# Kernel optimization log

Hardware: AMD Instinct MI355X
Metric: run time of the kernel (lower is better)

Reference implementation:

```python
import jax, jax.numpy as jnp
import numpy as np

NUM_HEAD = 8
D_MODEL = 512
HEAD_DIM = D_MODEL // NUM_HEAD
SCALING = HEAD_DIM ** (-0.5)
B, NQ, NK = 2, 2048, 2048


def setup_inputs() -> dict:
    key = jax.random.key(0)
    ks = jax.random.split(key, 12)
    s = 1.0 / np.sqrt(D_MODEL)
    return {
        "q": jax.random.normal(ks[0], (B, NQ, D_MODEL), jnp.float32),
        "k": jax.random.normal(ks[1], (B, NK, D_MODEL), jnp.float32),
        "v": jax.random.normal(ks[2], (B, NK, D_MODEL), jnp.float32),
        "mask_head": jax.random.uniform(ks[3], (B, NUM_HEAD, NQ, NK), jnp.float32),
        "pearson_matrix": jax.random.normal(ks[4], (B, NUM_HEAD, NK, NK), jnp.float32),
        "Wq": jax.random.uniform(ks[5], (D_MODEL, D_MODEL), jnp.float32, -s, s),
        "bq": jax.random.uniform(ks[6], (D_MODEL,), jnp.float32, -s, s),
        "Wk": jax.random.uniform(ks[7], (D_MODEL, D_MODEL), jnp.float32, -s, s),
        "bk": jax.random.uniform(ks[8], (D_MODEL,), jnp.float32, -s, s),
        "Wv": jax.random.uniform(ks[9], (D_MODEL, D_MODEL), jnp.float32, -s, s),
        "bv": jax.random.uniform(ks[10], (D_MODEL,), jnp.float32, -s, s),
    }


def _split_heads(x):
    b, n, _ = x.shape
    return x.reshape(b, n, NUM_HEAD, HEAD_DIM).transpose(0, 2, 1, 3)  # b h n d


def reference(q, k, v, mask_head, pearson_matrix, Wq, bq, Wk, bk, Wv, bv):
    queries = _split_heads(q @ Wq.T + bq)
    keys = _split_heads(k @ Wk.T + bk)
    values = _split_heads(v @ Wv.T + bv)
    energy = jnp.einsum('bhqd,bhkd->bhqk', queries, keys) * SCALING
    att = jax.nn.softmax(energy, axis=-1)
    att = att * mask_head
    # einsum 'bhqk,bhkk->bhqk' = multiply by diagonal of pearson over last two axes
    diag = jnp.diagonal(pearson_matrix, axis1=-2, axis2=-1)  # b h k
    att = att * diag[:, :, None, :]
    agg = jnp.einsum('bhqk,bhkd->bhqd', att, values)
    b, h, n, d = agg.shape
    return agg.transpose(0, 2, 1, 3).reshape(b, n, h * d)
```

## Files before the change

### kernel.cpp

```cpp
#include <hip/hip_runtime.h>

#define NUM_HEAD 8
#define D_MODEL  512
#define HEAD_DIM 64
#define NSEQ     2048
#define SCALE_LOG2E 0.18033688011112042f

typedef __attribute__((ext_vector_type(8))) short bf16x8;
typedef __attribute__((ext_vector_type(4))) float f32x4;

static __device__ __forceinline__ unsigned short f2bf(float f) {
    unsigned u = __builtin_bit_cast(unsigned, f);
    u += 0x7fffu + ((u >> 16) & 1u);
    return (unsigned short)(u >> 16);
}
static __device__ __forceinline__ float bf2f(unsigned short h) {
    unsigned u = ((unsigned)h) << 16;
    return __builtin_bit_cast(float, u);
}
static __device__ __forceinline__ unsigned pk2(float a, float b) {
    return (unsigned)f2bf(a) | ((unsigned)f2bf(b) << 16);
}

#define PSTR 40

__global__ __launch_bounds__(256) void proj_kernel(
    const float* __restrict__ X, const float* __restrict__ W,
    const float* __restrict__ bias, unsigned short* __restrict__ outp)
{
    __shared__ unsigned short lA[128 * PSTR];
    __shared__ unsigned short lB[64 * PSTR];

    const int tid  = threadIdx.x;
    const int lane = tid & 63, wid = tid >> 6;
    const int quad = lane >> 4, l15 = lane & 15;
    const int wm = (wid >> 1) * 64;
    const int wn = (wid & 1) * 32;
    const int m0 = blockIdx.x * 128, n0 = blockIdx.y * 64;

    f32x4 acc[4][2];
    const f32x4 zf = {0.f, 0.f, 0.f, 0.f};
#pragma unroll
    for (int mi = 0; mi < 4; mi++)
#pragma unroll
        for (int ni = 0; ni < 2; ni++) acc[mi][ni] = zf;

    const int arow = tid >> 1, akc = (tid & 1) * 16;
    const int brow = tid >> 2, bkc = (tid & 3) * 8;

    for (int k0 = 0; k0 < D_MODEL; k0 += 32) {
        const float* ap = X + (m0 + arow) * D_MODEL + k0 + akc;
        float4 a0 = *(const float4*)(ap);
        float4 a1 = *(const float4*)(ap + 4);
        float4 a2 = *(const float4*)(ap + 8);
        float4 a3 = *(const float4*)(ap + 12);
        uint4 w0, w1;
        w0.x = pk2(a0.x, a0.y); w0.y = pk2(a0.z, a0.w);
        w0.z = pk2(a1.x, a1.y); w0.w = pk2(a1.z, a1.w);
        w1.x = pk2(a2.x, a2.y); w1.y = pk2(a2.z, a2.w);
        w1.z = pk2(a3.x, a3.y); w1.w = pk2(a3.z, a3.w);
        *(uint4*)&lA[arow * PSTR + akc]     = w0;
        *(uint4*)&lA[arow * PSTR + akc + 8] = w1;
        const float* bp = W + (n0 + brow) * D_MODEL + k0 + bkc;
        float4 b0 = *(const float4*)(bp);
        float4 b1 = *(const float4*)(bp + 4);
        uint4 wb;
        wb.x = pk2(b0.x, b0.y); wb.y = pk2(b0.z, b0.w);
        wb.z = pk2(b1.x, b1.y); wb.w = pk2(b1.z, b1.w);
        *(uint4*)&lB[brow * PSTR + bkc] = wb;
        __syncthreads();

        bf16x8 aF[4], bF[2];
#pragma unroll
        for (int mi = 0; mi < 4; mi++)
            aF[mi] = *(const bf16x8*)&lA[(wm + mi * 16 + l15) * PSTR + quad * 8];
#pragma unroll
        for (int ni = 0; ni < 2; ni++)
            bF[ni] = *(const bf16x8*)&lB[(wn + ni * 16 + l15) * PSTR + quad * 8];
#pragma unroll
        for (int mi = 0; mi < 4; mi++)
#pragma unroll
            for (int ni = 0; ni < 2; ni++)
                acc[mi][ni] = __builtin_amdgcn_mfma_f32_16x16x32_bf16(
                    aF[mi], bF[ni], acc[mi][ni], 0, 0, 0);
        __syncthreads();
    }

    const float bv0 = bias[n0 + wn + l15];
    const float bv1 = bias[n0 + wn + 16 + l15];
#pragma unroll
    for (int mi = 0; mi < 4; mi++) {
        const int mbase = m0 + wm + mi * 16 + quad * 4;
#pragma unroll
        for (int ni = 0; ni < 2; ni++) {
            const int c = n0 + wn + ni * 16 + l15;
            const int h = c >> 6, d = c & 63;
            const float bb_add = ni ? bv1 : bv0;
#pragma unroll
            for (int r = 0; r < 4; r++) {
                const int mm = mbase + r;
                const int bb = mm >> 11, n = mm & 2047;
                const float val = acc[mi][ni][r] + bb_add;
                outp[((bb * NUM_HEAD + h) * NSEQ + n) * HEAD_DIM + d] = f2bf(val);
            }
        }
    }
}

__global__ void diag_kernel(const float* __restrict__ pearson,
                            float* __restrict__ diag)
{
    const int t = blockIdx.x * blockDim.x + threadIdx.x;
    const int bh = t >> 11, kk = t & 2047;
    diag[t] = pearson[((size_t)(bh * NSEQ + kk)) * NSEQ + kk];
}

#define VSTR 72

__global__ __launch_bounds__(256) void attn_kernel(
    const unsigned short* __restrict__ Qp, const unsigned short* __restrict__ Kp,
    const unsigned short* __restrict__ Vp, const float* __restrict__ diag,
    const float* __restrict__ mask, float* __restrict__ out)
{
    __shared__ unsigned short lVt[64 * VSTR];
    __shared__ unsigned short lP[64 * VSTR];

    const int tid  = threadIdx.x;
    const int lane = tid & 63, wid = tid >> 6;
    const int quad = lane >> 4, l15 = lane & 15;
    const int bh = blockIdx.y;
    const int q0 = blockIdx.x * 64;

    const unsigned short* Qb = Qp + (size_t)bh * NSEQ * HEAD_DIM;
    const unsigned short* Kb = Kp + (size_t)bh * NSEQ * HEAD_DIM;
    const unsigned short* Vb = Vp + (size_t)bh * NSEQ * HEAD_DIM;
    const float* maskb = mask + (size_t)bh * NSEQ * NSEQ + (size_t)q0 * NSEQ;
    const float* diagb = diag + bh * NSEQ;

    bf16x8 qF[2];
    {
        const unsigned short* qp = Qb + (q0 + wid * 16 + l15) * HEAD_DIM + quad * 8;
        qF[0] = *(const bf16x8*)qp;
        qF[1] = *(const bf16x8*)(qp + 32);
    }

    const f32x4 zf = {0.f, 0.f, 0.f, 0.f};
    f32x4 oacc[4] = {zf, zf, zf, zf};
    float lacc[4] = {0.f, 0.f, 0.f, 0.f};

    const int vrow = tid >> 2;
    const int vdb  = (tid & 3) * 16;

    for (int kt = 0; kt < NSEQ; kt += 64) {
        bf16x8 kF[4][2];
#pragma unroll
        for (int nt = 0; nt < 4; nt++) {
            const unsigned short* kp = Kb + (kt + nt * 16 + l15) * HEAD_DIM + quad * 8;
            kF[nt][0] = *(const bf16x8*)kp;
            kF[nt][1] = *(const bf16x8*)(kp + 32);
        }
        float mv[4][4];
#pragma unroll
        for (int cf = 0; cf < 4; cf++)
#pragma unroll
            for (int r = 0; r < 4; r++)
                mv[cf][r] = maskb[(size_t)(wid * 16 + quad * 4 + r) * NSEQ + kt + cf * 16 + l15];

        {
            const float dg = diagb[kt + vrow];
            const unsigned short* vp = Vb + (kt + vrow) * HEAD_DIM + vdb;
            union { uint4 u; unsigned short s[8]; } va, vb2;
            va.u  = *(const uint4*)vp;
            vb2.u = *(const uint4*)(vp + 8);
#pragma unroll
            for (int i = 0; i < 8; i++) {
                lVt[(vdb + i) * VSTR + vrow]     = f2bf(bf2f(va.s[i]) * dg);
                lVt[(vdb + 8 + i) * VSTR + vrow] = f2bf(bf2f(vb2.s[i]) * dg);
            }
        }

        f32x4 sacc[4];
#pragma unroll
        for (int nt = 0; nt < 4; nt++) {
            sacc[nt] = __builtin_amdgcn_mfma_f32_16x16x32_bf16(qF[0], kF[nt][0], zf, 0, 0, 0);
            sacc[nt] = __builtin_amdgcn_mfma_f32_16x16x32_bf16(qF[1], kF[nt][1], sacc[nt], 0, 0, 0);
        }

#pragma unroll
        for (int cf = 0; cf < 4; cf++) {
#pragma unroll
            for (int r = 0; r < 4; r++) {
                const float p = __builtin_amdgcn_exp2f(sacc[cf][r] * SCALE_LOG2E);
                lacc[r] += p;
                lP[(wid * 16 + quad * 4 + r) * VSTR + cf * 16 + l15] = f2bf(p * mv[cf][r]);
            }
        }
        __syncthreads();

#pragma unroll
        for (int ks = 0; ks < 2; ks++) {
            const bf16x8 aP = *(const bf16x8*)&lP[(wid * 16 + l15) * VSTR + ks * 32 + quad * 8];
#pragma unroll
            for (int nt = 0; nt < 4; nt++) {
                const bf16x8 bV = *(const bf16x8*)&lVt[(nt * 16 + l15) * VSTR + ks * 32 + quad * 8];
                oacc[nt] = __builtin_amdgcn_mfma_f32_16x16x32_bf16(aP, bV, oacc[nt], 0, 0, 0);
            }
        }
        __syncthreads();
    }

#pragma unroll
    for (int r = 0; r < 4; r++) {
        float v = lacc[r];
        v += __shfl_xor(v, 1);
        v += __shfl_xor(v, 2);
        v += __shfl_xor(v, 4);
        v += __shfl_xor(v, 8);
        lacc[r] = v;
    }

    const int b = bh >> 3, h = bh & 7;
#pragma unroll
    for (int nt = 0; nt < 4; nt++)
#pragma unroll
        for (int r = 0; r < 4; r++) {
            const int qrow = q0 + wid * 16 + quad * 4 + r;
            out[((size_t)b * NSEQ + qrow) * D_MODEL + h * HEAD_DIM + nt * 16 + l15] =
                oacc[nt][r] / lacc[r];
        }
}

extern "C" void kernel_launch(void* const* d_in, const int* in_sizes, int n_in,
                              void* d_out, int out_size, void* d_ws, size_t ws_size,
                              hipStream_t stream) {
    const float* q       = (const float*)d_in[0];
    const float* k       = (const float*)d_in[1];
    const float* v       = (const float*)d_in[2];
    const float* mask    = (const float*)d_in[3];
    const float* pearson = (const float*)d_in[4];
    const float* Wq      = (const float*)d_in[5];
    const float* bq      = (const float*)d_in[6];
    const float* Wk      = (const float*)d_in[7];
    const float* bk      = (const float*)d_in[8];
    const float* Wv      = (const float*)d_in[9];
    const float* bv      = (const float*)d_in[10];

    unsigned short* Qp = (unsigned short*)d_ws;
    unsigned short* Kp = Qp + 2097152;
    unsigned short* Vp = Kp + 2097152;
    float* diag = (float*)((char*)d_ws + 12582912);
    float* out = (float*)d_out;

    proj_kernel<<<dim3(32, 8), 256, 0, stream>>>(q, Wq, bq, Qp);
    proj_kernel<<<dim3(32, 8), 256, 0, stream>>>(k, Wk, bk, Kp);
    proj_kernel<<<dim3(32, 8), 256, 0, stream>>>(v, Wv, bv, Vp);
    diag_kernel<<<dim3(128), 256, 0, stream>>>(pearson, diag);
    attn_kernel<<<dim3(32, 16), 256, 0, stream>>>(Qp, Kp, Vp, diag, mask, out);
}
```

Before: 588.8 us.

## Merge projections, pre-transpose V, drop LDS V staging and block barriers

Merges the three projection launches into one 3D grid, folds the softmax scale into Q, and has the V projection write a transposed layout so attention reads V fragments straight from global memory. Mask and diagonal are now loaded as vectors with nontemporal hints and applied to the P fragment after it is read back, which removes both __syncthreads per tile because each wave only touches its own lP rows. Output stores become nontemporal. The cost is extra register pressure and strided transposed writes in the projection, plus an added bf16 rounding step on P before the mask multiply.

```diff
diff --git a/kernel.cpp b/kernel.cpp
--- a/kernel.cpp
+++ b/kernel.cpp
@@ -8,6 +8,7 @@
 
 typedef __attribute__((ext_vector_type(8))) short bf16x8;
 typedef __attribute__((ext_vector_type(4))) float f32x4;
+typedef __attribute__((ext_vector_type(4))) float vf4;
 
 static __device__ __forceinline__ unsigned short f2bf(float f) {
     unsigned u = __builtin_bit_cast(unsigned, f);
@@ -24,12 +25,20 @@
 
 #define PSTR 40
 
-__global__ __launch_bounds__(256) void proj_kernel(
-    const float* __restrict__ X, const float* __restrict__ W,
-    const float* __restrict__ bias, unsigned short* __restrict__ outp)
+__global__ __launch_bounds__(256) void proj3_kernel(
+    const float* __restrict__ Xq, const float* __restrict__ Xk, const float* __restrict__ Xv,
+    const float* __restrict__ Wq, const float* __restrict__ Wk, const float* __restrict__ Wv,
+    const float* __restrict__ bq, const float* __restrict__ bk, const float* __restrict__ bv,
+    unsigned short* __restrict__ Qp, unsigned short* __restrict__ Kp,
+    unsigned short* __restrict__ Vt)
 {
     __shared__ unsigned short lA[128 * PSTR];
     __shared__ unsigned short lB[64 * PSTR];
+
+    const int z = blockIdx.z;
+    const float* X    = (z == 0) ? Xq : (z == 1) ? Xk : Xv;
+    const float* W    = (z == 0) ? Wq : (z == 1) ? Wk : Wv;
+    const float* bias = (z == 0) ? bq : (z == 1) ? bk : bv;
 
     const int tid  = threadIdx.x;
     const int lane = tid & 63, wid = tid >> 6;
@@ -86,8 +95,10 @@
         __syncthreads();
     }
 
+    const float oscale = (z == 0) ? SCALE_LOG2E : 1.0f;
     const float bv0 = bias[n0 + wn + l15];
     const float bv1 = bias[n0 + wn + 16 + l15];
+    unsigned short* outp = (z == 0) ? Qp : Kp;
 #pragma unroll
     for (int mi = 0; mi < 4; mi++) {
         const int mbase = m0 + wm + mi * 16 + quad * 4;
@@ -100,8 +111,11 @@
             for (int r = 0; r < 4; r++) {
                 const int mm = mbase + r;
                 const int bb = mm >> 11, n = mm & 2047;
-                const float val = acc[mi][ni][r] + bb_add;
-                outp[((bb * NUM_HEAD + h) * NSEQ + n) * HEAD_DIM + d] = f2bf(val);
+                const float val = (acc[mi][ni][r] + bb_add) * oscale;
+                if (z < 2)
+                    outp[((bb * NUM_HEAD + h) * NSEQ + n) * HEAD_DIM + d] = f2bf(val);
+                else
+                    Vt[((bb * NUM_HEAD + h) * HEAD_DIM + d) * NSEQ + n] = f2bf(val);
             }
         }
     }
@@ -112,17 +126,17 @@
 {
     const int t = blockIdx.x * blockDim.x + threadIdx.x;
     const int bh = t >> 11, kk = t & 2047;
-    diag[t] = pearson[((size_t)(bh * NSEQ + kk)) * NSEQ + kk];
-}
-
-#define VSTR 72
+    diag[t] = __builtin_nontemporal_load(
+        pearson + ((size_t)(bh * NSEQ + kk)) * NSEQ + kk);
+}
+
+#define VSTR 68
 
 __global__ __launch_bounds__(256) void attn_kernel(
     const unsigned short* __restrict__ Qp, const unsigned short* __restrict__ Kp,
-    const unsigned short* __restrict__ Vp, const float* __restrict__ diag,
+    const unsigned short* __restrict__ Vt, const float* __restrict__ diag,
     const float* __restrict__ mask, float* __restrict__ out)
 {
-    __shared__ unsigned short lVt[64 * VSTR];
     __shared__ unsigned short lP[64 * VSTR];
 
     const int tid  = threadIdx.x;
@@ -131,11 +145,12 @@
     const int bh = blockIdx.y;
     const int q0 = blockIdx.x * 64;
 
-    const unsigned short* Qb = Qp + (size_t)bh * NSEQ * HEAD_DIM;
-    const unsigned short* Kb = Kp + (size_t)bh * NSEQ * HEAD_DIM;
-    const unsigned short* Vb = Vp + (size_t)bh * NSEQ * HEAD_DIM;
-    const float* maskb = mask + (size_t)bh * NSEQ * NSEQ + (size_t)q0 * NSEQ;
-    const float* diagb = diag + bh * NSEQ;
+    const unsigned short* Qb  = Qp + (size_t)bh * NSEQ * HEAD_DIM;
+    const unsigned short* Kb  = Kp + (size_t)bh * NSEQ * HEAD_DIM;
+    const unsigned short* Vtb = Vt + (size_t)bh * HEAD_DIM * NSEQ;
+    const float* mrow  = mask + (size_t)bh * NSEQ * NSEQ
+                              + (size_t)(q0 + wid * 16 + l15) * NSEQ + quad * 8;
+    const float* diagb = diag + bh * NSEQ + quad * 8;
 
     bf16x8 qF[2];
     {
@@ -148,8 +163,8 @@
     f32x4 oacc[4] = {zf, zf, zf, zf};
     float lacc[4] = {0.f, 0.f, 0.f, 0.f};
 
-    const int vrow = tid >> 2;
-    const int vdb  = (tid & 3) * 16;
+    const int lpw = (wid * 16 + quad * 4) * VSTR + l15;
+    const int lpr = (wid * 16 + l15) * VSTR + quad * 8;
 
     for (int kt = 0; kt < NSEQ; kt += 64) {
         bf16x8 kF[4][2];
@@ -159,24 +174,20 @@
             kF[nt][0] = *(const bf16x8*)kp;
             kF[nt][1] = *(const bf16x8*)(kp + 32);
         }
-        float mv[4][4];
-#pragma unroll
-        for (int cf = 0; cf < 4; cf++)
-#pragma unroll
-            for (int r = 0; r < 4; r++)
-                mv[cf][r] = maskb[(size_t)(wid * 16 + quad * 4 + r) * NSEQ + kt + cf * 16 + l15];
-
-        {
-            const float dg = diagb[kt + vrow];
-            const unsigned short* vp = Vb + (kt + vrow) * HEAD_DIM + vdb;
-            union { uint4 u; unsigned short s[8]; } va, vb2;
-            va.u  = *(const uint4*)vp;
-            vb2.u = *(const uint4*)(vp + 8);
-#pragma unroll
-            for (int i = 0; i < 8; i++) {
-                lVt[(vdb + i) * VSTR + vrow]     = f2bf(bf2f(va.s[i]) * dg);
-                lVt[(vdb + 8 + i) * VSTR + vrow] = f2bf(bf2f(vb2.s[i]) * dg);
-            }
+        bf16x8 vF[2][4];
+#pragma unroll
+        for (int ks = 0; ks < 2; ks++)
+#pragma unroll
+            for (int nt = 0; nt < 4; nt++)
+                vF[ks][nt] = *(const bf16x8*)&Vtb[(nt * 16 + l15) * NSEQ
+                                                  + kt + ks * 32 + quad * 8];
+        vf4 mA[4], dA[4];
+#pragma unroll
+        for (int ks = 0; ks < 2; ks++) {
+            mA[2 * ks]     = __builtin_nontemporal_load((const vf4*)(mrow + kt + ks * 32));
+            mA[2 * ks + 1] = __builtin_nontemporal_load((const vf4*)(mrow + kt + ks * 32 + 4));
+            dA[2 * ks]     = *(const vf4*)(diagb + kt + ks * 32);
+            dA[2 * ks + 1] = *(const vf4*)(diagb + kt + ks * 32 + 4);
         }
 
         f32x4 sacc[4];
@@ -187,26 +198,28 @@
         }
 
 #pragma unroll
-        for (int cf = 0; cf < 4; cf++) {
+        for (int cf = 0; cf < 4; cf++)
 #pragma unroll
             for (int r = 0; r < 4; r++) {
-                const float p = __builtin_amdgcn_exp2f(sacc[cf][r] * SCALE_LOG2E);
+                const float p = __builtin_amdgcn_exp2f(sacc[cf][r]);
                 lacc[r] += p;
-                lP[(wid * 16 + quad * 4 + r) * VSTR + cf * 16 + l15] = f2bf(p * mv[cf][r]);
+                lP[lpw + r * VSTR + cf * 16] = f2bf(p);
             }
-        }
-        __syncthreads();
 
 #pragma unroll
         for (int ks = 0; ks < 2; ks++) {
-            const bf16x8 aP = *(const bf16x8*)&lP[(wid * 16 + l15) * VSTR + ks * 32 + quad * 8];
-#pragma unroll
-            for (int nt = 0; nt < 4; nt++) {
-                const bf16x8 bV = *(const bf16x8*)&lVt[(nt * 16 + l15) * VSTR + ks * 32 + quad * 8];
-                oacc[nt] = __builtin_amdgcn_mfma_f32_16x16x32_bf16(aP, bV, oacc[nt], 0, 0, 0);
+            const bf16x8 aP = *(const bf16x8*)&lP[lpr + ks * 32];
+            bf16x8 aM;
+#pragma unroll
+            for (int j = 0; j < 8; j++) {
+                const float mj = (j < 4) ? mA[2 * ks][j] : mA[2 * ks + 1][j - 4];
+                const float dj = (j < 4) ? dA[2 * ks][j] : dA[2 * ks + 1][j - 4];
+                aM[j] = (short)f2bf(bf2f((unsigned short)aP[j]) * mj * dj);
             }
-        }
-        __syncthreads();
+#pragma unroll
+            for (int nt = 0; nt < 4; nt++)
+                oacc[nt] = __builtin_amdgcn_mfma_f32_16x16x32_bf16(aM, vF[ks][nt], oacc[nt], 0, 0, 0);
+        }
     }
 
 #pragma unroll
@@ -225,8 +238,9 @@
 #pragma unroll
         for (int r = 0; r < 4; r++) {
             const int qrow = q0 + wid * 16 + quad * 4 + r;
-            out[((size_t)b * NSEQ + qrow) * D_MODEL + h * HEAD_DIM + nt * 16 + l15] =
-                oacc[nt][r] / lacc[r];
+            __builtin_nontemporal_store(
+                oacc[nt][r] / lacc[r],
+                out + ((size_t)b * NSEQ + qrow) * D_MODEL + h * HEAD_DIM + nt * 16 + l15);
         }
 }
 
@@ -247,13 +261,12 @@
 
     unsigned short* Qp = (unsigned short*)d_ws;
     unsigned short* Kp = Qp + 2097152;
-    unsigned short* Vp = Kp + 2097152;
+    unsigned short* Vtp = Kp + 2097152;
     float* diag = (float*)((char*)d_ws + 12582912);
     float* out = (float*)d_out;
 
-    proj_kernel<<<dim3(32, 8), 256, 0, stream>>>(q, Wq, bq, Qp);
-    proj_kernel<<<dim3(32, 8), 256, 0, stream>>>(k, Wk, bk, Kp);
-    proj_kernel<<<dim3(32, 8), 256, 0, stream>>>(v, Wv, bv, Vp);
+    proj3_kernel<<<dim3(32, 8, 3), 256, 0, stream>>>(q, k, v, Wq, Wk, Wv,
+                                                     bq, bk, bv, Qp, Kp, Vtp);
     diag_kernel<<<dim3(128), 256, 0, stream>>>(pearson, diag);
-    attn_kernel<<<dim3(32, 16), 256, 0, stream>>>(Qp, Kp, Vp, diag, mask, out);
-}
+    attn_kernel<<<dim3(32, 16), 256, 0, stream>>>(Qp, Kp, Vtp, diag, mask, out);
+}
```

New measurement: 655.7 us. 1.11x slower.
